# Optimization experiments

Hardware: AMD Instinct MI355X
Metric: run time of the kernel (lower is better)

Reference implementation:

```python
import jax, jax.numpy as jnp
import numpy as np

K_CURV = 1.0   # Lorentz(k=1.0)
EPS = 1e-6


def _project(space):
    # lift space components onto hyperboloid: t = sqrt(k + ||s||^2)
    t = jnp.sqrt(K_CURV + jnp.sum(space * space, axis=-1, keepdims=True))
    return jnp.concatenate([t, space], axis=-1)


def setup_inputs():
    key = jax.random.key(0)
    B, N, D, H = 4, 1024, 128, 8
    ks = jax.random.split(key, 7)
    # valid Lorentz points: [B, N, D] with x[...,0] the time coordinate
    x = _project(jax.random.normal(ks[0], (B, N, D - 1), dtype=jnp.float32) * 0.5)
    scale = 1.0 / np.sqrt(D)
    Wq = jax.random.normal(ks[1], (H, D - 1, D), dtype=jnp.float32) * scale
    Wk = jax.random.normal(ks[2], (H, D - 1, D), dtype=jnp.float32) * scale
    Wv = jax.random.normal(ks[3], (H, D - 1, D), dtype=jnp.float32) * scale
    bq = jnp.zeros((H, D - 1), dtype=jnp.float32)
    bk = jnp.zeros((H, D - 1), dtype=jnp.float32)
    bv = jnp.zeros((H, D - 1), dtype=jnp.float32)
    beta = jnp.ones((H,), dtype=jnp.float32)
    gamma = jnp.zeros((H,), dtype=jnp.float32)
    return {"x": x, "Wq": Wq, "bq": bq, "Wk": Wk, "bk": bk, "Wv": Wv, "bv": bv,
            "beta": beta, "gamma": gamma}


def _lorentz_fc(x, W, b):
    # HyboNet-style Lorentz fully-connected (identity activation), all heads at once.
    # x: [B,N,D], W: [H,D-1,D], b: [H,D-1] -> [H,B,N,D] on the hyperboloid
    space = jnp.einsum('bnd,hed->hbne', x, W) + b[:, None, None, :]
    return _project(space)


def reference(x, Wq, bq, Wk, bk, Wv, bv, beta, gamma):
    D = x.shape[-1]
    sign = jnp.concatenate([-jnp.ones((1,), x.dtype), jnp.ones((D - 1,), x.dtype)])
    Q = _lorentz_fc(x, Wq, bq)   # [H,B,N,D]
    K = _lorentz_fc(x, Wk, bk)
    V = _lorentz_fc(x, Wv, bv)
    # pairwise Minkowski inner product <q,k>_L = -t_q t_k + s_q . s_k
    inner = jnp.einsum('hbid,hbjd->hbij', Q * sign, K)          # [H,B,N,N]
    dists = jnp.arccosh(jnp.maximum(-inner / K_CURV, 1.0 + EPS)) * np.sqrt(K_CURV)
    scores = -beta[:, None, None, None] * dists - gamma[:, None, None, None]
    attn = jax.nn.softmax(scores, axis=-1)
    # Lorentz midpoint: normalize weighted sum back onto the hyperboloid
    mid = jnp.einsum('hbij,hbjd->hbid', attn, V)                # [H,B,N,D]
    mnorm = jnp.einsum('hbid,hbid->hbi', mid * sign, mid)       # <m,m>_L (negative)
    head_out = mid * (np.sqrt(K_CURV) / jnp.sqrt(jnp.maximum(-mnorm, EPS)))[..., None]
    # direct_concat: concatenate space parts, recompute time coordinate
    H = head_out.shape[0]
    t = head_out[..., 0]                                        # [H,B,N]
    s = jnp.moveaxis(head_out[..., 1:], 0, 2)                   # [B,N,H,D-1]
    space_cat = s.reshape(s.shape[0], s.shape[1], -1)           # [B,N,H*(D-1)]
    time = jnp.sqrt(jnp.maximum(jnp.sum(t * t, axis=0) - (H - 1) * K_CURV, EPS))
    return jnp.concatenate([time[..., None], space_cat], axis=-1)  # [B,N,H*(D-1)+1]
```

## Files before the change

kernel.cpp:

```cpp
#include <hip/hip_runtime.h>

typedef __attribute__((ext_vector_type(8))) short short8_t;
typedef __attribute__((ext_vector_type(4))) short short4_t;
typedef __attribute__((ext_vector_type(4))) float float4_t;
typedef __attribute__((ext_vector_type(2))) unsigned int uint2_t;

__device__ __forceinline__ unsigned short f2bf(float f) {
    unsigned u = __builtin_bit_cast(unsigned, f);
    u += 0x7FFFu + ((u >> 16) & 1u);
    return (unsigned short)(u >> 16);
}

__device__ __forceinline__ unsigned pk_bf16(float a, float b) {
    unsigned r;
    asm("v_cvt_pk_bf16_f32 %0, %1, %2" : "=v"(r) : "v"(a), "v"(b));
    return r;
}

#define MFMA(A, B, C) __builtin_amdgcn_mfma_f32_16x16x32_bf16((A), (B), (C), 0, 0, 0)

__global__ __launch_bounds__(256) void k_proj(
    const float* __restrict__ x,
    const float* __restrict__ Wq, const float* __restrict__ bq,
    const float* __restrict__ Wk, const float* __restrict__ bk,
    const float* __restrict__ Wv, const float* __restrict__ bv,
    unsigned short* __restrict__ Qs, unsigned short* __restrict__ Kb,
    unsigned short* __restrict__ Vt)
{
    __shared__ __align__(16) unsigned char lds[17408 + 34816 + 1024];
    unsigned short* Xs  = (unsigned short*)lds;
    unsigned short* Ws  = (unsigned short*)(lds + 17408);
    float*          ssqB = (float*)(lds + 17408 + 34816);
    unsigned short* Ot  = Ws;
    unsigned short* OtT = Ws;

    const int tid = threadIdx.x;
    const int m0  = blockIdx.x * 64;
    const int h   = blockIdx.y;
    const int mat = blockIdx.z;
    const float* W  = (mat == 0) ? Wq : ((mat == 1) ? Wk : Wv);
    const float* bb = (mat == 0) ? bq : ((mat == 1) ? bk : bv);

    #pragma unroll
    for (int p = 0; p < 8; p++) {
        int r = p * 8 + (tid >> 5), c = (tid & 31) * 4;
        float4_t v = *(const float4_t*)(x + (m0 + r) * 128 + c);
        uint2_t u; u[0] = pk_bf16(v[0], v[1]); u[1] = pk_bf16(v[2], v[3]);
        *(uint2_t*)(Xs + r * 136 + c) = u;
    }
    #pragma unroll
    for (int p = 0; p < 16; p++) {
        int e = p * 8 + (tid >> 5), c = (tid & 31) * 4;
        float4_t v = {0.f, 0.f, 0.f, 0.f};
        if (e < 127) v = *(const float4_t*)(W + (h * 127 + e) * 128 + c);
        uint2_t u; u[0] = pk_bf16(v[0], v[1]); u[1] = pk_bf16(v[2], v[3]);
        *(uint2_t*)(Ws + e * 136 + c) = u;
    }
    __syncthreads();

    const int w = tid >> 6, lane = tid & 63, li = lane & 15, lg = lane >> 4;
    float4_t acc[4][2];
    #pragma unroll
    for (int i = 0; i < 4; i++)
        #pragma unroll
        for (int j = 0; j < 2; j++) acc[i][j] = (float4_t){0.f, 0.f, 0.f, 0.f};

    #pragma unroll
    for (int kk = 0; kk < 4; kk++) {
        short8_t Bf[2];
        #pragma unroll
        for (int ni = 0; ni < 2; ni++)
            Bf[ni] = *(short8_t*)(Ws + (w * 32 + ni * 16 + li) * 136 + kk * 32 + lg * 8);
        #pragma unroll
        for (int mi = 0; mi < 4; mi++) {
            short8_t A = *(short8_t*)(Xs + (mi * 16 + li) * 136 + kk * 32 + lg * 8);
            #pragma unroll
            for (int ni = 0; ni < 2; ni++) acc[mi][ni] = MFMA(A, Bf[ni], acc[mi][ni]);
        }
    }
    #pragma unroll
    for (int ni = 0; ni < 2; ni++) {
        int e = w * 32 + ni * 16 + li;
        float bvv = (e < 127) ? bb[h * 127 + e] : 0.0f;
        #pragma unroll
        for (int mi = 0; mi < 4; mi++)
            #pragma unroll
            for (int r = 0; r < 4; r++) acc[mi][ni][r] += bvv;
    }
    #pragma unroll
    for (int mi = 0; mi < 4; mi++) {
        #pragma unroll
        for (int r = 0; r < 4; r++) {
            float s = acc[mi][0][r] * acc[mi][0][r] + acc[mi][1][r] * acc[mi][1][r];
            s += __shfl_xor(s, 1);  s += __shfl_xor(s, 2);
            s += __shfl_xor(s, 4);  s += __shfl_xor(s, 8);
            if (li == 0) ssqB[(mi * 16 + lg * 4 + r) * 4 + w] = s;
        }
    }
    __syncthreads();

    if (mat < 2) {
        #pragma unroll
        for (int mi = 0; mi < 4; mi++)
            #pragma unroll
            for (int ni = 0; ni < 2; ni++) {
                int e = w * 32 + ni * 16 + li;
                if (e < 127) {
                    #pragma unroll
                    for (int r = 0; r < 4; r++)
                        Ot[(mi * 16 + lg * 4 + r) * 136 + 1 + e] = f2bf(acc[mi][ni][r]);
                }
            }
        if (tid < 64) {
            float s = ssqB[tid * 4] + ssqB[tid * 4 + 1] + ssqB[tid * 4 + 2] + ssqB[tid * 4 + 3];
            float t = sqrtf(1.0f + s);
            Ot[tid * 136] = f2bf(mat == 0 ? -t : t);
        }
        __syncthreads();
        unsigned short* dst = ((mat == 0) ? Qs : Kb) + (h * 4096 + m0) * 128;
        #pragma unroll
        for (int p = 0; p < 4; p++) {
            int r = p * 16 + (tid >> 4), c = (tid & 15) * 8;
            *(short8_t*)(dst + r * 128 + c) = *(short8_t*)(Ot + r * 136 + c);
        }
    } else {
        #pragma unroll
        for (int mi = 0; mi < 4; mi++)
            #pragma unroll
            for (int ni = 0; ni < 2; ni++) {
                int e = w * 32 + ni * 16 + li;
                if (e < 127) {
                    uint2_t u;
                    u[0] = pk_bf16(acc[mi][ni][0], acc[mi][ni][1]);
                    u[1] = pk_bf16(acc[mi][ni][2], acc[mi][ni][3]);
                    *(uint2_t*)(OtT + (1 + e) * 72 + mi * 16 + lg * 4) = u;
                }
            }
        if (tid < 64) {
            float s = ssqB[tid * 4] + ssqB[tid * 4 + 1] + ssqB[tid * 4 + 2] + ssqB[tid * 4 + 3];
            OtT[tid] = f2bf(sqrtf(1.0f + s));
        }
        __syncthreads();
        int b = m0 >> 10, n0 = m0 & 1023;
        unsigned short* dst = Vt + (h * 4 + b) * 131072 + n0;
        #pragma unroll
        for (int p = 0; p < 4; p++) {
            int d = p * 32 + (tid >> 3), nc = (tid & 7) * 8;
            *(short8_t*)(dst + d * 1024 + nc) = *(short8_t*)(OtT + d * 72 + nc);
        }
    }
}

__global__ __launch_bounds__(256, 2) void k_attn(
    const unsigned short* __restrict__ Qsg, const unsigned short* __restrict__ Kb,
    const unsigned short* __restrict__ Vt,
    const float* __restrict__ beta, const float* __restrict__ gamma,
    float* __restrict__ out, float* __restrict__ tsq)
{
    __shared__ __align__(16) unsigned char lds[80896];
    unsigned short* Kbuf0 = (unsigned short*)lds;
    unsigned short* Kbuf1 = (unsigned short*)(lds + 17408);
    unsigned short* Vbuf0 = (unsigned short*)(lds + 34816);
    unsigned short* Vbuf1 = (unsigned short*)(lds + 53248);
    unsigned short* Ps    = (unsigned short*)(lds + 71680);
    float*          ow    = (float*)lds;

    const int tid = threadIdx.x, w = tid >> 6, lane = tid & 63;
    const int li = lane & 15, lg = lane >> 4;

    const int bid = blockIdx.x;
    const int hb = (bid & 7) * 4 + (bid >> 7);
    const int qt = (bid >> 3) & 15;
    const int h = hb >> 2, b = hb & 3;
    const int q0 = qt * 64;

    const unsigned short* Qp = Qsg + (h * 4096 + b * 1024) * 128;
    const unsigned short* Kp = Kb  + (h * 4096 + b * 1024) * 128;
    const unsigned short* Vp = Vt  + (h * 4 + b) * 131072;
    const float bet = beta[h];
    const bool beta1 = (bet == 1.0f);
    (void)gamma;

    const int kr = tid >> 4, kc = (tid & 15) * 8;
    const int vd = tid >> 3, vc = (tid & 7) * 8;
    const unsigned short* Kld = Kp + kr * 128 + kc;
    const unsigned short* Vld = Vp + vd * 1024 + vc;

    short8_t qf[4];
    const int qrow = q0 + w * 16 + li;
    #pragma unroll
    for (int kk = 0; kk < 4; kk++)
        qf[kk] = *(const short8_t*)(Qp + qrow * 128 + kk * 32 + lg * 8);

    float4_t amid[8];
    #pragma unroll
    for (int df = 0; df < 8; df++) amid[df] = (float4_t){0.f, 0.f, 0.f, 0.f};
    float m = -INFINITY, lsum = 0.0f;

    short8_t kreg[4], vreg[4];
    #pragma unroll
    for (int p = 0; p < 4; p++) {
        kreg[p] = *(const short8_t*)(Kld + p * 2048);
        vreg[p] = *(const short8_t*)(Vld + p * 32768);
    }
    #pragma unroll
    for (int p = 0; p < 4; p++) {
        *(short8_t*)(Kbuf0 + (p * 16 + kr) * 136 + kc) = kreg[p];
        *(short8_t*)(Vbuf0 + (p * 32 + vd) * 72 + vc) = vreg[p];
    }
    __syncthreads();

    for (int t = 0; t < 16; t++) {
        unsigned short* Kc = (t & 1) ? Kbuf1 : Kbuf0;
        unsigned short* Vc = (t & 1) ? Vbuf1 : Vbuf0;
        unsigned short* Kn = (t & 1) ? Kbuf0 : Kbuf1;
        unsigned short* Vn = (t & 1) ? Vbuf0 : Vbuf1;

        if (t < 15) {
            const int j0n = (t + 1) * 64;
            #pragma unroll
            for (int p = 0; p < 4; p++) {
                kreg[p] = *(const short8_t*)(Kld + j0n * 128 + p * 2048);
                vreg[p] = *(const short8_t*)(Vld + p * 32768 + j0n);
            }
        }
        __builtin_amdgcn_sched_barrier(0);

        float4_t as[4];
        #pragma unroll
        for (int jf = 0; jf < 4; jf++) as[jf] = (float4_t){0.f, 0.f, 0.f, 0.f};
        __builtin_amdgcn_s_setprio(1);
        #pragma unroll
        for (int kk = 0; kk < 4; kk++) {
            #pragma unroll
            for (int jf = 0; jf < 4; jf++) {
                short8_t A = *(short8_t*)(Kc + (jf * 16 + li) * 136 + kk * 32 + lg * 8);
                as[jf] = MFMA(A, qf[kk], as[jf]);
            }
        }
        __builtin_amdgcn_s_setprio(0);

        float ps_ = 0.0f;
        if (beta1) {
            #pragma unroll
            for (int jf = 0; jf < 4; jf++) {
                float p[4];
                #pragma unroll
                for (int r = 0; r < 4; r++) {
                    float z = fmaxf(-as[jf][r], 1.0f + 1e-6f);
                    float wv = z + __builtin_amdgcn_sqrtf(__builtin_fmaf(z, z, -1.0f));
                    p[r] = __builtin_amdgcn_rcpf(wv);
                    ps_ += p[r];
                }
                uint2_t u; u[0] = pk_bf16(p[0], p[1]); u[1] = pk_bf16(p[2], p[3]);
                *(uint2_t*)(Ps + (w * 16 + li) * 72 + jf * 16 + lg * 4) = u;
            }
        } else {
            float s2[16];
            float tm = -INFINITY;
            #pragma unroll
            for (int jf = 0; jf < 4; jf++) {
                #pragma unroll
                for (int r = 0; r < 4; r++) {
                    float z = fmaxf(-as[jf][r], 1.0f + 1e-6f);
                    float wv = z + __builtin_amdgcn_sqrtf(__builtin_fmaf(z, z, -1.0f));
                    float s = -bet * __builtin_amdgcn_logf(wv);
                    s2[jf * 4 + r] = s;
                    tm = fmaxf(tm, s);
                }
            }
            tm = fmaxf(tm, __shfl_xor(tm, 16));
            tm = fmaxf(tm, __shfl_xor(tm, 32));
            if (__any(tm > m + 8.0f)) {
                float mn = fmaxf(m, tm);
                float scale = __builtin_amdgcn_exp2f(m - mn);
                lsum *= scale;
                #pragma unroll
                for (int df = 0; df < 8; df++)
                    #pragma unroll
                    for (int r = 0; r < 4; r++) amid[df][r] *= scale;
                m = mn;
            }
            #pragma unroll
            for (int jf = 0; jf < 4; jf++) {
                float p0 = __builtin_amdgcn_exp2f(s2[jf * 4 + 0] - m);
                float p1 = __builtin_amdgcn_exp2f(s2[jf * 4 + 1] - m);
                float p2 = __builtin_amdgcn_exp2f(s2[jf * 4 + 2] - m);
                float p3 = __builtin_amdgcn_exp2f(s2[jf * 4 + 3] - m);
                ps_ += (p0 + p1) + (p2 + p3);
                uint2_t u; u[0] = pk_bf16(p0, p1); u[1] = pk_bf16(p2, p3);
                *(uint2_t*)(Ps + (w * 16 + li) * 72 + jf * 16 + lg * 4) = u;
            }
        }
        ps_ += __shfl_xor(ps_, 16);
        ps_ += __shfl_xor(ps_, 32);
        lsum += ps_;
        asm volatile("s_waitcnt lgkmcnt(0)" ::: "memory");
        __builtin_amdgcn_sched_barrier(0);

        __builtin_amdgcn_s_setprio(1);
        #pragma unroll
        for (int kk2 = 0; kk2 < 2; kk2++) {
            short8_t Bp = *(short8_t*)(Ps + (w * 16 + li) * 72 + kk2 * 32 + lg * 8);
            #pragma unroll
            for (int df = 0; df < 8; df++) {
                short8_t A = *(short8_t*)(Vc + (df * 16 + li) * 72 + kk2 * 32 + lg * 8);
                amid[df] = MFMA(A, Bp, amid[df]);
            }
        }
        __builtin_amdgcn_s_setprio(0);

        if (t < 15) {
            #pragma unroll
            for (int p = 0; p < 4; p++) {
                *(short8_t*)(Kn + (p * 16 + kr) * 136 + kc) = kreg[p];
                *(short8_t*)(Vn + (p * 32 + vd) * 72 + vc) = vreg[p];
            }
        }
        __syncthreads();
    }

    float invl = 1.0f / lsum;
    float ssq = 0.0f;
    #pragma unroll
    for (int df = 0; df < 8; df++) {
        #pragma unroll
        for (int r = 0; r < 4; r++) {
            float v = amid[df][r] * invl;
            amid[df][r] = v;
            ssq += v * v;
        }
    }
    ssq += __shfl_xor(ssq, 16);
    ssq += __shfl_xor(ssq, 32);
    float tmid = __shfl(amid[0][0], li);
    float denom = fmaxf(2.0f * tmid * tmid - ssq, 1e-6f);
    float rs = 1.0f / sqrtf(denom);

    #pragma unroll
    for (int df = 0; df < 8; df++) {
        #pragma unroll
        for (int r = 0; r < 4; r++)
            ow[w * 2112 + li * 132 + df * 16 + lg * 4 + r] = amid[df][r] * rs;
    }
    asm volatile("s_waitcnt lgkmcnt(0)" ::: "memory");
    __builtin_amdgcn_sched_barrier(0);

    #pragma unroll
    for (int i = 0; i < 16; i++) {
        int n = q0 + w * 16 + i;
        float v0 = ow[w * 2112 + i * 132 + lane];
        float v1 = ow[w * 2112 + i * 132 + 64 + lane];
        float* orow = out + (b * 1024 + n) * 1017;
        if (lane == 0) tsq[h * 4096 + b * 1024 + n] = v0 * v0;
        else           orow[h * 127 + lane] = v0;
        orow[h * 127 + 64 + lane] = v1;
    }
}

__global__ __launch_bounds__(256) void k_time(const float* __restrict__ tsq,
                                              float* __restrict__ out)
{
    int mrow = blockIdx.x * 256 + threadIdx.x;
    float s = 0.0f;
    #pragma unroll
    for (int h = 0; h < 8; h++) s += tsq[h * 4096 + mrow];
    out[mrow * 1017] = sqrtf(fmaxf(s - 7.0f, 1e-6f));
}

extern "C" void kernel_launch(void* const* d_in, const int* in_sizes, int n_in,
                              void* d_out, int out_size, void* d_ws, size_t ws_size,
                              hipStream_t stream)
{
    const float* x    = (const float*)d_in[0];
    const float* Wq   = (const float*)d_in[1];
    const float* bq   = (const float*)d_in[2];
    const float* Wk   = (const float*)d_in[3];
    const float* bk   = (const float*)d_in[4];
    const float* Wv   = (const float*)d_in[5];
    const float* bv   = (const float*)d_in[6];
    const float* beta = (const float*)d_in[7];
    const float* gam  = (const float*)d_in[8];
    float* out = (float*)d_out;

    unsigned char* ws = (unsigned char*)d_ws;
    unsigned short* Qs = (unsigned short*)(ws);
    unsigned short* Kb = (unsigned short*)(ws + 8388608);
    unsigned short* Vt = (unsigned short*)(ws + 16777216);
    float*          ts = (float*)(ws + 25165824);

    k_proj<<<dim3(64, 8, 3), 256, 0, stream>>>(x, Wq, bq, Wk, bk, Wv, bv, Qs, Kb, Vt);
    k_attn<<<dim3(512), 256, 0, stream>>>(Qs, Kb, Vt, beta, gam, out, ts);
    k_time<<<dim3(16), 256, 0, stream>>>(ts, out);
}
```

Before: 136.7 us.

## Cut LDS use to raise occupancy in projection and attention kernels

```diff
diff --git a/kernel.cpp b/kernel.cpp
--- a/kernel.cpp
+++ b/kernel.cpp
@@ -17,9 +17,16 @@
     return r;
 }
 
+__device__ __forceinline__ short8_t pk8(float4_t a, float4_t b) {
+    union { unsigned u[4]; short8_t s; } r;
+    r.u[0] = pk_bf16(a[0], a[1]); r.u[1] = pk_bf16(a[2], a[3]);
+    r.u[2] = pk_bf16(b[0], b[1]); r.u[3] = pk_bf16(b[2], b[3]);
+    return r.s;
+}
+
 #define MFMA(A, B, C) __builtin_amdgcn_mfma_f32_16x16x32_bf16((A), (B), (C), 0, 0, 0)
 
-__global__ __launch_bounds__(256) void k_proj(
+__global__ __launch_bounds__(256, 4) void k_proj(
     const float* __restrict__ x,
     const float* __restrict__ Wq, const float* __restrict__ bq,
     const float* __restrict__ Wk, const float* __restrict__ bk,
@@ -27,12 +34,11 @@
     unsigned short* __restrict__ Qs, unsigned short* __restrict__ Kb,
     unsigned short* __restrict__ Vt)
 {
-    __shared__ __align__(16) unsigned char lds[17408 + 34816 + 1024];
+    __shared__ __align__(16) unsigned char lds[19456];
     unsigned short* Xs  = (unsigned short*)lds;
-    unsigned short* Ws  = (unsigned short*)(lds + 17408);
-    float*          ssqB = (float*)(lds + 17408 + 34816);
-    unsigned short* Ot  = Ws;
-    unsigned short* OtT = Ws;
+    unsigned short* Ot  = (unsigned short*)lds;
+    unsigned short* OtT = (unsigned short*)lds;
+    float*          ssqB = (float*)(lds + 18432);
 
     const int tid = threadIdx.x;
     const int m0  = blockIdx.x * 64;
@@ -41,6 +47,23 @@
     const float* W  = (mat == 0) ? Wq : ((mat == 1) ? Wk : Wv);
     const float* bb = (mat == 0) ? bq : ((mat == 1) ? bk : bv);
 
+    const int w = tid >> 6, lane = tid & 63, li = lane & 15, lg = lane >> 4;
+
+    const int e = w * 32 + li;
+    float4_t wf[8][2];
+    #pragma unroll
+    for (int ni = 0; ni < 2; ni++) {
+        int ee = e + ni * 16;
+        const float* wp = W + (h * 127 + (ee < 127 ? ee : 0)) * 128 + lg * 8;
+        #pragma unroll
+        for (int kk = 0; kk < 4; kk++) {
+            float4_t a = *(const float4_t*)(wp + kk * 32);
+            float4_t b2 = *(const float4_t*)(wp + kk * 32 + 4);
+            if (ee >= 127) { a = (float4_t){0.f,0.f,0.f,0.f}; b2 = (float4_t){0.f,0.f,0.f,0.f}; }
+            wf[ni * 4 + kk][0] = a; wf[ni * 4 + kk][1] = b2;
+        }
+    }
+
     #pragma unroll
     for (int p = 0; p < 8; p++) {
         int r = p * 8 + (tid >> 5), c = (tid & 31) * 4;
@@ -48,17 +71,12 @@
         uint2_t u; u[0] = pk_bf16(v[0], v[1]); u[1] = pk_bf16(v[2], v[3]);
         *(uint2_t*)(Xs + r * 136 + c) = u;
     }
-    #pragma unroll
-    for (int p = 0; p < 16; p++) {
-        int e = p * 8 + (tid >> 5), c = (tid & 31) * 4;
-        float4_t v = {0.f, 0.f, 0.f, 0.f};
-        if (e < 127) v = *(const float4_t*)(W + (h * 127 + e) * 128 + c);
-        uint2_t u; u[0] = pk_bf16(v[0], v[1]); u[1] = pk_bf16(v[2], v[3]);
-        *(uint2_t*)(Ws + e * 136 + c) = u;
-    }
     __syncthreads();
 
-    const int w = tid >> 6, lane = tid & 63, li = lane & 15, lg = lane >> 4;
+    short8_t Bf[8];
+    #pragma unroll
+    for (int f = 0; f < 8; f++) Bf[f] = pk8(wf[f][0], wf[f][1]);
+
     float4_t acc[4][2];
     #pragma unroll
     for (int i = 0; i < 4; i++)
@@ -67,21 +85,17 @@
 
     #pragma unroll
     for (int kk = 0; kk < 4; kk++) {
-        short8_t Bf[2];
-        #pragma unroll
-        for (int ni = 0; ni < 2; ni++)
-            Bf[ni] = *(short8_t*)(Ws + (w * 32 + ni * 16 + li) * 136 + kk * 32 + lg * 8);
         #pragma unroll
         for (int mi = 0; mi < 4; mi++) {
             short8_t A = *(short8_t*)(Xs + (mi * 16 + li) * 136 + kk * 32 + lg * 8);
-            #pragma unroll
-            for (int ni = 0; ni < 2; ni++) acc[mi][ni] = MFMA(A, Bf[ni], acc[mi][ni]);
+            acc[mi][0] = MFMA(A, Bf[kk],     acc[mi][0]);
+            acc[mi][1] = MFMA(A, Bf[4 + kk], acc[mi][1]);
         }
     }
     #pragma unroll
     for (int ni = 0; ni < 2; ni++) {
-        int e = w * 32 + ni * 16 + li;
-        float bvv = (e < 127) ? bb[h * 127 + e] : 0.0f;
+        int ee = e + ni * 16;
+        float bvv = (ee < 127) ? bb[h * 127 + ee] : 0.0f;
         #pragma unroll
         for (int mi = 0; mi < 4; mi++)
             #pragma unroll
@@ -104,11 +118,11 @@
         for (int mi = 0; mi < 4; mi++)
             #pragma unroll
             for (int ni = 0; ni < 2; ni++) {
-                int e = w * 32 + ni * 16 + li;
-                if (e < 127) {
+                int ee = e + ni * 16;
+                if (ee < 127) {
                     #pragma unroll
                     for (int r = 0; r < 4; r++)
-                        Ot[(mi * 16 + lg * 4 + r) * 136 + 1 + e] = f2bf(acc[mi][ni][r]);
+                        Ot[(mi * 16 + lg * 4 + r) * 136 + 1 + ee] = f2bf(acc[mi][ni][r]);
                 }
             }
         if (tid < 64) {
@@ -128,12 +142,12 @@
         for (int mi = 0; mi < 4; mi++)
             #pragma unroll
             for (int ni = 0; ni < 2; ni++) {
-                int e = w * 32 + ni * 16 + li;
-                if (e < 127) {
+                int ee = e + ni * 16;
+                if (ee < 127) {
                     uint2_t u;
                     u[0] = pk_bf16(acc[mi][ni][0], acc[mi][ni][1]);
                     u[1] = pk_bf16(acc[mi][ni][2], acc[mi][ni][3]);
-                    *(uint2_t*)(OtT + (1 + e) * 72 + mi * 16 + lg * 4) = u;
+                    *(uint2_t*)(OtT + (1 + ee) * 72 + mi * 16 + lg * 4) = u;
                 }
             }
         if (tid < 64) {
@@ -151,19 +165,17 @@
     }
 }
 
-__global__ __launch_bounds__(256, 2) void k_attn(
+__global__ __launch_bounds__(256, 3) void k_attn(
     const unsigned short* __restrict__ Qsg, const unsigned short* __restrict__ Kb,
     const unsigned short* __restrict__ Vt,
     const float* __restrict__ beta, const float* __restrict__ gamma,
     float* __restrict__ out, float* __restrict__ tsq)
 {
-    __shared__ __align__(16) unsigned char lds[80896];
-    unsigned short* Kbuf0 = (unsigned short*)lds;
-    unsigned short* Kbuf1 = (unsigned short*)(lds + 17408);
-    unsigned short* Vbuf0 = (unsigned short*)(lds + 34816);
-    unsigned short* Vbuf1 = (unsigned short*)(lds + 53248);
-    unsigned short* Ps    = (unsigned short*)(lds + 71680);
-    float*          ow    = (float*)lds;
+    __shared__ __align__(16) unsigned char lds[45056];
+    unsigned short* Ks  = (unsigned short*)lds;
+    unsigned short* Vts = (unsigned short*)(lds + 17408);
+    unsigned short* Ps  = (unsigned short*)(lds + 35840);
+    float*          ow  = (float*)lds;
 
     const int tid = threadIdx.x, w = tid >> 6, lane = tid & 63;
     const int li = lane & 15, lg = lane >> 4;
@@ -205,17 +217,12 @@
     }
     #pragma unroll
     for (int p = 0; p < 4; p++) {
-        *(short8_t*)(Kbuf0 + (p * 16 + kr) * 136 + kc) = kreg[p];
-        *(short8_t*)(Vbuf0 + (p * 32 + vd) * 72 + vc) = vreg[p];
+        *(short8_t*)(Ks  + (p * 16 + kr) * 136 + kc) = kreg[p];
+        *(short8_t*)(Vts + (p * 32 + vd) * 72 + vc) = vreg[p];
     }
     __syncthreads();
 
     for (int t = 0; t < 16; t++) {
-        unsigned short* Kc = (t & 1) ? Kbuf1 : Kbuf0;
-        unsigned short* Vc = (t & 1) ? Vbuf1 : Vbuf0;
-        unsigned short* Kn = (t & 1) ? Kbuf0 : Kbuf1;
-        unsigned short* Vn = (t & 1) ? Vbuf0 : Vbuf1;
-
         if (t < 15) {
             const int j0n = (t + 1) * 64;
             #pragma unroll
@@ -234,7 +241,7 @@
         for (int kk = 0; kk < 4; kk++) {
             #pragma unroll
             for (int jf = 0; jf < 4; jf++) {
-                short8_t A = *(short8_t*)(Kc + (jf * 16 + li) * 136 + kk * 32 + lg * 8);
+                short8_t A = *(short8_t*)(Ks + (jf * 16 + li) * 136 + kk * 32 + lg * 8);
                 as[jf] = MFMA(A, qf[kk], as[jf]);
             }
         }
@@ -304,20 +311,21 @@
             short8_t Bp = *(short8_t*)(Ps + (w * 16 + li) * 72 + kk2 * 32 + lg * 8);
             #pragma unroll
             for (int df = 0; df < 8; df++) {
-                short8_t A = *(short8_t*)(Vc + (df * 16 + li) * 72 + kk2 * 32 + lg * 8);
+                short8_t A = *(short8_t*)(Vts + (df * 16 + li) * 72 + kk2 * 32 + lg * 8);
                 amid[df] = MFMA(A, Bp, amid[df]);
             }
         }
         __builtin_amdgcn_s_setprio(0);
 
         if (t < 15) {
+            __syncthreads();
             #pragma unroll
             for (int p = 0; p < 4; p++) {
-                *(short8_t*)(Kn + (p * 16 + kr) * 136 + kc) = kreg[p];
-                *(short8_t*)(Vn + (p * 32 + vd) * 72 + vc) = vreg[p];
-            }
-        }
-        __syncthreads();
+                *(short8_t*)(Ks  + (p * 16 + kr) * 136 + kc) = kreg[p];
+                *(short8_t*)(Vts + (p * 32 + vd) * 72 + vc) = vreg[p];
+            }
+            __syncthreads();
+        }
     }
 
     float invl = 1.0f / lsum;
@@ -337,6 +345,7 @@
     float denom = fmaxf(2.0f * tmid * tmid - ssq, 1e-6f);
     float rs = 1.0f / sqrtf(denom);
 
+    __syncthreads();
     #pragma unroll
     for (int df = 0; df < 8; df++) {
         #pragma unroll
```

Result: no change. 137.8 us (+0.8%).
